# Performance work log

Hardware: AMD Instinct MI355X
Metric: run time of the kernel (lower is better)

## Reference

```python
import jax, jax.numpy as jnp
import numpy as np

NUM_EMBEDDINGS = 1024
EMBEDDING_DIM = 32  # Z_NH
COMMITMENT_LOSS_FACTOR = 0.1
QUANTIZATION_LOSS_FACTOR = 0.1


def setup_inputs() -> dict:
    key = jax.random.key(0)
    k1, k2 = jax.random.split(key)
    h = jax.random.normal(k1, (256, 512, EMBEDDING_DIM), dtype=jnp.float32)
    # nn.Embedding weight init: uniform(-1/K, 1/K)
    embeddings = jax.random.uniform(
        k2, (NUM_EMBEDDINGS, EMBEDDING_DIM), dtype=jnp.float32,
        minval=-1.0 / NUM_EMBEDDINGS, maxval=1.0 / NUM_EMBEDDINGS)
    return {"h": h, "embeddings": embeddings}


def reference(h, embeddings):
    flat = h.reshape(-1, EMBEDDING_DIM)                       # [N, D]
    dist = ((flat ** 2).sum(-1, keepdims=True)
            + (embeddings ** 2).sum(-1)
            - 2.0 * flat @ embeddings.T)                      # [N, K]
    idx = jnp.argmin(dist, axis=-1)                           # [N]
    # one_hot @ weight == direct row gather
    quantized = embeddings[idx].reshape(h.shape)              # [B, S, D]
    q_flat = quantized.reshape(-1, EMBEDDING_DIM)
    commitment_loss = jnp.mean((jax.lax.stop_gradient(q_flat) - flat) ** 2, axis=-1)
    embedding_loss = jnp.mean((q_flat - jax.lax.stop_gradient(flat)) ** 2, axis=-1)
    # straight-through estimator
    quantized_st = h + jax.lax.stop_gradient(quantized - h)
    loss = (commitment_loss * COMMITMENT_LOSS_FACTOR
            + embedding_loss * QUANTIZATION_LOSS_FACTOR)      # [N]
    quantized_indices = idx[:, None]                          # [N, 1]
    return quantized_st, quantized_indices, loss
```

## Files before the change

kernel.cpp:

```cpp
#include <hip/hip_runtime.h>


#define EMB_N 1024
#define DIM 32
#define NVEC (256 * 512)
#define NTILES (EMB_N / 16)
#define NT_LDS 36
#define MAXC 8

typedef unsigned long long u64;
typedef unsigned int u32;
typedef unsigned short ushortT;
typedef __attribute__((ext_vector_type(8))) short bf16x8;
typedef __attribute__((ext_vector_type(4))) float f32x4;

__device__ __forceinline__ u32 enc_f32(float x) {
    u32 u = __float_as_uint(x);
    return (u & 0x80000000u) ? ~u : (u | 0x80000000u);
}
__device__ __forceinline__ ushortT f2bf(float f) {
    u32 u = __float_as_uint(f);
    return (ushortT)((u + 0x7FFFu + ((u >> 16) & 1u)) >> 16);
}
__device__ __forceinline__ u64 shflx_u64(u64 x, int m) {
    int lo = __shfl_xor((int)(u32)x, m);
    int hi = __shfl_xor((int)(x >> 32), m);
    return ((u64)(u32)hi << 32) | (u32)lo;
}

__device__ __forceinline__ float norm2_np(const float* fr) {
    float sq[DIM];
#pragma unroll
    for (int i = 0; i < DIM; ++i) sq[i] = fr[i] * fr[i];
    float r[8];
#pragma unroll
    for (int j = 0; j < 8; ++j)
        r[j] = ((sq[j] + sq[j + 8]) + sq[j + 16]) + sq[j + 24];
    return ((r[0] + r[1]) + (r[2] + r[3])) + ((r[4] + r[5]) + (r[6] + r[7]));
}

__global__ __launch_bounds__(256) void prep_kernel(
    const float* __restrict__ emb, float* __restrict__ e2,
    ushortT* __restrict__ bfrag)
{
#pragma clang fp contract(off)
    const int t = blockIdx.x * 256 + threadIdx.x;
    const int l = t & 63;
    const int row = ((t >> 6) << 4) + (l & 15);
    const int k0 = (l >> 4) * 8;
    const float* ep = emb + (size_t)row * DIM + k0;
    ushortT* dst = bfrag + (size_t)t * 8;
#pragma unroll
    for (int j = 0; j < 8; ++j) dst[j] = f2bf(ep[j]);
    if (t < EMB_N) {
        const float* e = emb + (size_t)t * DIM;
        float tmp[DIM];
#pragma unroll
        for (int i = 0; i < DIM; ++i) tmp[i] = e[i];
        e2[t] = norm2_np(tmp);
    }
}

#define S1BODY(BEXPR) do {                                                      \
    bf16x8 b = *(const bf16x8*)(BEXPR);                                         \
    f32x4 d0 = __builtin_amdgcn_mfma_f32_16x16x32_bf16(afr0, b, zacc, 0, 0, 0); \
    f32x4 d1 = __builtin_amdgcn_mfma_f32_16x16x32_bf16(afr1, b, zacc, 0, 0, 0); \
    _Pragma("unroll")                                                           \
    for (int r = 0; r < 4; ++r) {                                               \
        bs[r]     = fmaxf(bs[r],     d0[r]);                                    \
        bs[4 + r] = fmaxf(bs[4 + r], d1[r]);                                    \
    }                                                                           \
} while (0)

#define S2BODY(BEXPR, NT) do {                                                  \
    bf16x8 b = *(const bf16x8*)(BEXPR);                                         \
    f32x4 d0 = __builtin_amdgcn_mfma_f32_16x16x32_bf16(afr0, b, zacc, 0, 0, 0); \
    f32x4 d1 = __builtin_amdgcn_mfma_f32_16x16x32_bf16(afr1, b, zacc, 0, 0, 0); \
    const u32 cc = (NT) * 16 + col16;                                           \
    bool q[8];                                                                  \
    bool any = false;                                                           \
    _Pragma("unroll")                                                           \
    for (int i = 0; i < 8; ++i) {                                               \
        float dv = ((i >> 2) ? d1[i & 3] : d0[i & 3]);                          \
        q[i] = (dv >= thr[i]);                                                  \
        any |= q[i];                                                            \
    }                                                                           \
    if (__ballot(any)) {                                                        \
        _Pragma("unroll")                                                       \
        for (int i = 0; i < 8; ++i) {                                           \
            if (__ballot(q[i])) {                                               \
                if (q[i]) {                                                     \
                    const int rloc = ((i >> 2) << 4) + quad * 4 + (i & 3);      \
                    u32 slot = atomicAdd(&cnt[rloc], 1u);                       \
                    if (slot < MAXC) cand[rloc * MAXC + slot] = (ushortT)cc;    \
                }                                                               \
            }                                                                   \
        }                                                                       \
    }                                                                           \
} while (0)

__global__ __launch_bounds__(256) void vq_scan(
    const float* __restrict__ h,
    const float* __restrict__ emb,
    const float* __restrict__ e2,
    const ushortT* __restrict__ bfrag,
    float* __restrict__ out_q, float* __restrict__ out_idx,
    float* __restrict__ out_loss)
{
#pragma clang fp contract(off)
    __shared__ __align__(16) ushortT s_b[NT_LDS * 512];
    __shared__ u32     lds_cnt[4][32];
    __shared__ ushortT lds_cand[4][32 * MAXC];

    {
        const uint4* src = (const uint4*)bfrag;
        uint4* dst = (uint4*)s_b;
        for (int o = threadIdx.x; o < NT_LDS * 64; o += 256) dst[o] = src[o];
    }

    const int wslot = threadIdx.x >> 6;
    const int wid   = (blockIdx.x * 256 + threadIdx.x) >> 6;
    const int lane  = threadIdx.x & 63;
    const int col16 = lane & 15;
    const int quad  = lane >> 4;
    const size_t row0 = (size_t)wid * 32;

    u32*     cnt  = lds_cnt[wslot];
    ushortT* cand = lds_cand[wslot];
    if (lane < 32) cnt[lane] = 0;

    bf16x8 afr0, afr1;
    float sa0, sa1;
    {
        const float* ap = h + (row0 + col16) * DIM + quad * 8;
        float4 x = *(const float4*)ap, y = *(const float4*)(ap + 4);
        afr0[0]=(short)f2bf(x.x); afr0[1]=(short)f2bf(x.y); afr0[2]=(short)f2bf(x.z); afr0[3]=(short)f2bf(x.w);
        afr0[4]=(short)f2bf(y.x); afr0[5]=(short)f2bf(y.y); afr0[6]=(short)f2bf(y.z); afr0[7]=(short)f2bf(y.w);
        sa0 = fabsf(x.x)+fabsf(x.y)+fabsf(x.z)+fabsf(x.w)+fabsf(y.x)+fabsf(y.y)+fabsf(y.z)+fabsf(y.w);
        const float* bp = ap + 16 * DIM;
        float4 u = *(const float4*)bp, v = *(const float4*)(bp + 4);
        afr1[0]=(short)f2bf(u.x); afr1[1]=(short)f2bf(u.y); afr1[2]=(short)f2bf(u.z); afr1[3]=(short)f2bf(u.w);
        afr1[4]=(short)f2bf(v.x); afr1[5]=(short)f2bf(v.y); afr1[6]=(short)f2bf(v.z); afr1[7]=(short)f2bf(v.w);
        sa1 = fabsf(u.x)+fabsf(u.y)+fabsf(u.z)+fabsf(u.w)+fabsf(v.x)+fabsf(v.y)+fabsf(v.z)+fabsf(v.w);
    }
    sa0 += __shfl_xor(sa0, 16); sa0 += __shfl_xor(sa0, 32);
    sa1 += __shfl_xor(sa1, 16); sa1 += __shfl_xor(sa1, 32);

    __syncthreads();

    const f32x4 zacc = {0.f, 0.f, 0.f, 0.f};

    float bs[8];
#pragma unroll
    for (int i = 0; i < 8; ++i) bs[i] = -3.4e38f;
#pragma unroll 2
    for (int nt = 0; nt < NT_LDS; ++nt)
        S1BODY(s_b + nt * 512 + lane * 8);
#pragma unroll 2
    for (int nt = NT_LDS; nt < NTILES; ++nt)
        S1BODY(bfrag + nt * 512 + lane * 8);
#pragma unroll
    for (int m = 1; m < 16; m <<= 1)
#pragma unroll
        for (int i = 0; i < 8; ++i) bs[i] = fmaxf(bs[i], __shfl_xor(bs[i], m));

    float thr[8];
#pragma unroll
    for (int i = 0; i < 8; ++i) {
        float sar = __shfl((i >> 2) ? sa1 : sa0, quad * 4 + (i & 3));
        thr[i] = bs[i] - __builtin_fmaf(sar, 0x1p-16f, 1.0e-4f);
    }

#pragma unroll 2
    for (int nt = 0; nt < NT_LDS; ++nt)
        S2BODY(s_b + nt * 512 + lane * 8, nt);
#pragma unroll 2
    for (int nt = NT_LDS; nt < NTILES; ++nt)
        S2BODY(bfrag + nt * 512 + lane * 8, nt);

    u64 ovf = __ballot((lane < 32) && (cnt[lane & 31] > MAXC));
    while (ovf) {
        const int r = (int)(__ffsll((unsigned long long)ovf) - 1);
        ovf &= ovf - 1;
        const float* fp = h + (row0 + r) * DIM;
        float fu[DIM];
#pragma unroll
        for (int i = 0; i < DIM; i += 4) {
            float4 x = *(const float4*)(fp + i);
            fu[i] = x.x; fu[i + 1] = x.y; fu[i + 2] = x.z; fu[i + 3] = x.w;
        }
        const float f2 = norm2_np(fu);
        u64 bk = ~0ull;
        for (int c = lane; c < EMB_N; c += 64) {
            const float* ep = emb + (size_t)c * DIM;
            float a = 0.f;
#pragma unroll
            for (int k = 0; k < DIM; ++k) a = __builtin_fmaf(fu[k], ep[k], a);
            float dd = (f2 + e2[c]) - (2.0f * a);
            u64 key = ((u64)enc_f32(dd) << 32) | (u32)c;
            if (key < bk) bk = key;
        }
#pragma unroll
        for (int m = 1; m < 64; m <<= 1) {
            u64 o = shflx_u64(bk, m);
            if (o < bk) bk = o;
        }
        if (lane == 0) { cand[r * MAXC] = (ushortT)(bk & 1023u); cnt[r] = 1; }
    }

    if (lane < 32) {
        const int row = (int)row0 + lane;
        const u32 n = cnt[lane];
        const float* f = h + (size_t)row * DIM;
        float fr[DIM];
#pragma unroll
        for (int i = 0; i < DIM; i += 4) {
            float4 x = *(const float4*)(f + i);
            fr[i] = x.x; fr[i + 1] = x.y; fr[i + 2] = x.z; fr[i + 3] = x.w;
        }
        int bidx;
        if (n == 1) {
            bidx = (int)cand[lane * MAXC];
        } else {
            const float f2 = norm2_np(fr);
            u64 best = ~0ull;
            for (u32 j = 0; j < n; ++j) {
                const u32 c = (u32)cand[lane * MAXC + j];
                const float* ep = emb + (size_t)c * DIM;
                float a = 0.f;
#pragma unroll
                for (int k = 0; k < DIM; ++k) a = __builtin_fmaf(fr[k], ep[k], a);
                float dd = (f2 + e2[c]) - (2.0f * a);
                u64 key = ((u64)enc_f32(dd) << 32) | c;
                if (key < best) best = key;
            }
            bidx = (int)(best & 0xFFFFFFFFu);
        }

        const float* qv = emb + (size_t)bidx * DIM;
        float ps = 0.f;
#pragma unroll
        for (int i = 0; i < DIM; i += 4) {
            float4 qx; qx.x = qv[i]; qx.y = qv[i+1]; qx.z = qv[i+2]; qx.w = qv[i+3];
            float dx = qx.x - fr[i], dy = qx.y - fr[i+1], dz = qx.z - fr[i+2], dw = qx.w - fr[i+3];
            ps += dx * dx; ps += dy * dy; ps += dz * dz; ps += dw * dw;
            float4 o;
            o.x = fr[i]     + (qx.x - fr[i]);
            o.y = fr[i + 1] + (qx.y - fr[i + 1]);
            o.z = fr[i + 2] + (qx.z - fr[i + 2]);
            o.w = fr[i + 3] + (qx.w - fr[i + 3]);
            *(float4*)(out_q + (size_t)row * DIM + i) = o;
        }
        float m = ps * (1.0f / DIM);
        out_idx[row]  = (float)bidx;
        out_loss[row] = m * 0.1f + m * 0.1f;
    }
}

__global__ void e2_kernel(const float* __restrict__ emb, float* __restrict__ e2) {
#pragma clang fp contract(off)
    int c = blockIdx.x * blockDim.x + threadIdx.x;
    if (c >= EMB_N) return;
    const float* e = emb + (size_t)c * DIM;
    float tmp[DIM];
#pragma unroll
    for (int i = 0; i < DIM; ++i) tmp[i] = e[i];
    e2[c] = norm2_np(tmp);
}

__global__ __launch_bounds__(256) void vq_kernel(
    const float* __restrict__ h, const float* __restrict__ emb,
    const float* __restrict__ e2, float* __restrict__ out_q,
    float* __restrict__ out_idx, float* __restrict__ out_loss)
{
#pragma clang fp contract(off)
    const int v = blockIdx.x * blockDim.x + threadIdx.x;
    const float* f = h + (size_t)v * DIM;
    float fr[DIM];
#pragma unroll
    for (int i = 0; i < DIM; i += 4) {
        float4 x = *(const float4*)(f + i);
        fr[i] = x.x; fr[i + 1] = x.y; fr[i + 2] = x.z; fr[i + 3] = x.w;
    }
    const float f2 = norm2_np(fr);
    float best = 3.4e38f; int bidx = 0;
#pragma unroll 1
    for (int c = 0; c < EMB_N; ++c) {
        const float* e = emb + (size_t)c * DIM;
        float a0 = 0.f;
#pragma unroll
        for (int k = 0; k < DIM; ++k) a0 = __builtin_fmaf(fr[k], e[k], a0);
        float d0 = (f2 + e2[c]) - (2.0f * a0);
        if (d0 < best) { best = d0; bidx = c; }
    }
    const float* q = emb + (size_t)bidx * DIM;
    float ps = 0.f;
#pragma unroll
    for (int i = 0; i < DIM; i += 4) {
        float4 qx; qx.x = q[i]; qx.y = q[i+1]; qx.z = q[i+2]; qx.w = q[i+3];
        float dx = qx.x - fr[i], dy = qx.y - fr[i+1], dz = qx.z - fr[i+2], dw = qx.w - fr[i+3];
        ps += dx * dx; ps += dy * dy; ps += dz * dz; ps += dw * dw;
        float4 o;
        o.x = fr[i] + (qx.x - fr[i]); o.y = fr[i+1] + (qx.y - fr[i+1]);
        o.z = fr[i+2] + (qx.z - fr[i+2]); o.w = fr[i+3] + (qx.w - fr[i+3]);
        *(float4*)(out_q + (size_t)v * DIM + i) = o;
    }
    float m = ps * (1.0f / DIM);
    out_idx[v]  = (float)bidx;
    out_loss[v] = m * 0.1f + m * 0.1f;
}

extern "C" void kernel_launch(void* const* d_in, const int* in_sizes, int n_in,
                              void* d_out, int out_size, void* d_ws, size_t ws_size,
                              hipStream_t stream) {
    const float* h   = (const float*)d_in[0];
    const float* emb = (const float*)d_in[1];
    float* out = (float*)d_out;
    float* out_q    = out;
    float* out_idx  = out + (size_t)NVEC * DIM;
    float* out_loss = out + (size_t)NVEC * DIM + NVEC;

    float*   e2    = (float*)d_ws;
    ushortT* bfrag = (ushortT*)((char*)d_ws + 4096);
    const size_t need = 4096 + (size_t)EMB_N * DIM * sizeof(ushortT);

    if (ws_size >= need) {
        prep_kernel<<<16, 256, 0, stream>>>(emb, e2, bfrag);
        vq_scan<<<1024, 256, 0, stream>>>(h, emb, e2, bfrag,
                                          out_q, out_idx, out_loss);
    } else {
        e2_kernel<<<EMB_N / 256, 256, 0, stream>>>(emb, e2);
        vq_kernel<<<NVEC / 256, 256, 0, stream>>>(h, emb, e2, out_q, out_idx, out_loss);
    }
}
```

Baseline: 126.2 us.

## Fuse two-pass MFMA scan into single pass with per-lane candidate bitmasks

Replaces the two full passes over the codebook (one to find each row's best similarity, one to recompute and collect near-best candidates) with a single pass. Each lane keeps a running max and bitmasks of tiles that beat a progressively tightened threshold, refreshed periodically by a cross-lane reduction. Global-memory B fragments are software-prefetched two tiles ahead. This halves the MFMA work and fragment loads, at the cost of more registers, a tighter margin constant, and possible extra candidates collected from early, looser thresholds.

```diff
diff --git a/kernel.cpp b/kernel.cpp
--- a/kernel.cpp
+++ b/kernel.cpp
@@ -61,42 +61,35 @@
     }
 }
 
-#define S1BODY(BEXPR) do {                                                      \
-    bf16x8 b = *(const bf16x8*)(BEXPR);                                         \
-    f32x4 d0 = __builtin_amdgcn_mfma_f32_16x16x32_bf16(afr0, b, zacc, 0, 0, 0); \
-    f32x4 d1 = __builtin_amdgcn_mfma_f32_16x16x32_bf16(afr1, b, zacc, 0, 0, 0); \
-    _Pragma("unroll")                                                           \
-    for (int r = 0; r < 4; ++r) {                                               \
-        bs[r]     = fmaxf(bs[r],     d0[r]);                                    \
-        bs[4 + r] = fmaxf(bs[4 + r], d1[r]);                                    \
-    }                                                                           \
+#define SBODY(BVAL, MASK, BIT) do {                                                 \
+    f32x4 d0 = __builtin_amdgcn_mfma_f32_16x16x32_bf16(afr0, (BVAL), zacc, 0, 0, 0);\
+    f32x4 d1 = __builtin_amdgcn_mfma_f32_16x16x32_bf16(afr1, (BVAL), zacc, 0, 0, 0);\
+    _Pragma("unroll")                                                               \
+    for (int i = 0; i < 8; ++i) {                                                   \
+        float dv = (i >> 2) ? d1[i & 3] : d0[i & 3];                                \
+        MASK[i] |= (dv >= thr_s[i]) ? (BIT) : 0u;                                   \
+        bsloc[i] = fmaxf(bsloc[i], dv);                                             \
+    }                                                                               \
 } while (0)
 
-#define S2BODY(BEXPR, NT) do {                                                  \
-    bf16x8 b = *(const bf16x8*)(BEXPR);                                         \
-    f32x4 d0 = __builtin_amdgcn_mfma_f32_16x16x32_bf16(afr0, b, zacc, 0, 0, 0); \
-    f32x4 d1 = __builtin_amdgcn_mfma_f32_16x16x32_bf16(afr1, b, zacc, 0, 0, 0); \
-    const u32 cc = (NT) * 16 + col16;                                           \
-    bool q[8];                                                                  \
-    bool any = false;                                                           \
-    _Pragma("unroll")                                                           \
-    for (int i = 0; i < 8; ++i) {                                               \
-        float dv = ((i >> 2) ? d1[i & 3] : d0[i & 3]);                          \
-        q[i] = (dv >= thr[i]);                                                  \
-        any |= q[i];                                                            \
-    }                                                                           \
-    if (__ballot(any)) {                                                        \
-        _Pragma("unroll")                                                       \
-        for (int i = 0; i < 8; ++i) {                                           \
-            if (__ballot(q[i])) {                                               \
-                if (q[i]) {                                                     \
-                    const int rloc = ((i >> 2) << 4) + quad * 4 + (i & 3);      \
-                    u32 slot = atomicAdd(&cnt[rloc], 1u);                       \
-                    if (slot < MAXC) cand[rloc * MAXC + slot] = (ushortT)cc;    \
-                }                                                               \
-            }                                                                   \
-        }                                                                       \
-    }                                                                           \
+#define SLDS(NT, MASK, BIT) do {                                                    \
+    bf16x8 bql = *(const bf16x8*)(s_b + (NT) * 512 + lane * 8);                     \
+    SBODY(bql, MASK, BIT);                                                          \
+} while (0)
+
+#define SHARE() do {                                                                \
+    _Pragma("unroll")                                                               \
+    for (int i = 0; i < 8; ++i) {                                                   \
+        float t_ = bsloc[i];                                                        \
+        t_ = fmaxf(t_, __shfl_xor(t_, 1));                                          \
+        t_ = fmaxf(t_, __shfl_xor(t_, 2));                                          \
+        t_ = fmaxf(t_, __shfl_xor(t_, 4));                                          \
+        t_ = fmaxf(t_, __shfl_xor(t_, 8));                                          \
+        thr_s[i] = t_ - mg[i];                                                      \
+        bool keep_ = (bsloc[i] >= thr_s[i]);                                        \
+        ml[i] = keep_ ? ml[i] : 0u;                                                 \
+        mh[i] = keep_ ? mh[i] : 0u;                                                 \
+    }                                                                               \
 } while (0)
 
 __global__ __launch_bounds__(256) void vq_scan(
@@ -150,33 +143,63 @@
 
     const f32x4 zacc = {0.f, 0.f, 0.f, 0.f};
 
-    float bs[8];
-#pragma unroll
-    for (int i = 0; i < 8; ++i) bs[i] = -3.4e38f;
-#pragma unroll 2
-    for (int nt = 0; nt < NT_LDS; ++nt)
-        S1BODY(s_b + nt * 512 + lane * 8);
-#pragma unroll 2
-    for (int nt = NT_LDS; nt < NTILES; ++nt)
-        S1BODY(bfrag + nt * 512 + lane * 8);
-#pragma unroll
-    for (int m = 1; m < 16; m <<= 1)
-#pragma unroll
-        for (int i = 0; i < 8; ++i) bs[i] = fmaxf(bs[i], __shfl_xor(bs[i], m));
-
-    float thr[8];
+    float bsloc[8], thr_s[8], mg[8];
+    u32 ml[8], mh[8];
 #pragma unroll
     for (int i = 0; i < 8; ++i) {
+        bsloc[i] = -3.4e38f; thr_s[i] = -3.4e38f; ml[i] = 0u; mh[i] = 0u;
         float sar = __shfl((i >> 2) ? sa1 : sa0, quad * 4 + (i & 3));
-        thr[i] = bs[i] - __builtin_fmaf(sar, 0x1p-16f, 1.0e-4f);
-    }
-
-#pragma unroll 2
-    for (int nt = 0; nt < NT_LDS; ++nt)
-        S2BODY(s_b + nt * 512 + lane * 8, nt);
-#pragma unroll 2
-    for (int nt = NT_LDS; nt < NTILES; ++nt)
-        S2BODY(bfrag + nt * 512 + lane * 8, nt);
+        mg[i] = __builtin_fmaf(sar, 0x1.8p-17f, 4.0e-5f);
+    }
+
+    SLDS(0, ml, 1u);
+    SHARE();
+#pragma unroll
+    for (int nt = 1; nt < 16; ++nt) SLDS(nt, ml, 1u << nt);
+    SHARE();
+#pragma unroll
+    for (int nt = 16; nt < 32; ++nt) SLDS(nt, ml, 1u << nt);
+    SHARE();
+#pragma unroll
+    for (int nt = 32; nt < NT_LDS; ++nt) SLDS(nt, mh, 1u << (nt - 32));
+
+    bf16x8 p0 = *(const bf16x8*)(bfrag + 36 * 512 + lane * 8);
+    bf16x8 p1 = *(const bf16x8*)(bfrag + 37 * 512 + lane * 8);
+#pragma unroll
+    for (int nt = 36; nt < 48; ++nt) {
+        bf16x8 nx = *(const bf16x8*)(bfrag + (nt + 2) * 512 + lane * 8);
+        SBODY(p0, mh, 1u << (nt - 32));
+        p0 = p1; p1 = nx;
+    }
+    SHARE();
+#pragma unroll
+    for (int nt = 48; nt < 62; ++nt) {
+        bf16x8 nx = *(const bf16x8*)(bfrag + (nt + 2) * 512 + lane * 8);
+        SBODY(p0, mh, 1u << (nt - 32));
+        p0 = p1; p1 = nx;
+    }
+    SBODY(p0, mh, 1u << 30);
+    SBODY(p1, mh, 1u << 31);
+    SHARE();
+
+#pragma unroll
+    for (int i = 0; i < 8; ++i) {
+        if (bsloc[i] >= thr_s[i]) {
+            const int rloc = ((i >> 2) << 4) + quad * 4 + (i & 3);
+            u32 m0 = ml[i];
+            while (m0) {
+                int b = __ffs(m0) - 1; m0 &= m0 - 1;
+                u32 slot = atomicAdd(&cnt[rloc], 1u);
+                if (slot < MAXC) cand[rloc * MAXC + slot] = (ushortT)((b << 4) + col16);
+            }
+            u32 m1 = mh[i];
+            while (m1) {
+                int b = __ffs(m1) - 1; m1 &= m1 - 1;
+                u32 slot = atomicAdd(&cnt[rloc], 1u);
+                if (slot < MAXC) cand[rloc * MAXC + slot] = (ushortT)(((b + 32) << 4) + col16);
+            }
+        }
+    }
 
     u64 ovf = __ballot((lane < 32) && (cnt[lane & 31] > MAXC));
     while (ovf) {
```

Result: slower. 177.1 us (+40.4%).

## Split codebook scan across wave pairs and tighten candidate threshold

Applied to the files above, without the earlier changes.

Each 32-row group is now handled by two waves that take alternating codebook tiles, doubling the block size to 512 threads. The per-row maxima from the first pass are combined through shared memory, so each wave's MFMA work halves and latency is spread over more waves. The candidate-pruning margin is also narrowed, which should produce fewer exact re-check candidates. The narrower margin risks missing the true argmin when bf16 error exceeds the new bound, and the extra barriers plus the idle second wave during finalization add some overhead.

```diff
diff --git a/kernel.cpp b/kernel.cpp
--- a/kernel.cpp
+++ b/kernel.cpp
@@ -76,7 +76,7 @@
     bf16x8 b = *(const bf16x8*)(BEXPR);                                         \
     f32x4 d0 = __builtin_amdgcn_mfma_f32_16x16x32_bf16(afr0, b, zacc, 0, 0, 0); \
     f32x4 d1 = __builtin_amdgcn_mfma_f32_16x16x32_bf16(afr1, b, zacc, 0, 0, 0); \
-    const u32 cc = (NT) * 16 + col16;                                           \
+    const u32 cc = (u32)(NT) * 16 + col16;                                      \
     bool q[8];                                                                  \
     bool any = false;                                                           \
     _Pragma("unroll")                                                           \
@@ -99,7 +99,7 @@
     }                                                                           \
 } while (0)
 
-__global__ __launch_bounds__(256) void vq_scan(
+__global__ __launch_bounds__(512, 8) void vq_scan(
     const float* __restrict__ h,
     const float* __restrict__ emb,
     const float* __restrict__ e2,
@@ -109,25 +109,27 @@
 {
 #pragma clang fp contract(off)
     __shared__ __align__(16) ushortT s_b[NT_LDS * 512];
+    __shared__ float   sm[8][32];
     __shared__ u32     lds_cnt[4][32];
     __shared__ ushortT lds_cand[4][32 * MAXC];
 
     {
         const uint4* src = (const uint4*)bfrag;
         uint4* dst = (uint4*)s_b;
-        for (int o = threadIdx.x; o < NT_LDS * 64; o += 256) dst[o] = src[o];
+        for (int o = threadIdx.x; o < NT_LDS * 64; o += 512) dst[o] = src[o];
     }
 
     const int wslot = threadIdx.x >> 6;
-    const int wid   = (blockIdx.x * 256 + threadIdx.x) >> 6;
+    const int pair  = wslot >> 1;
+    const int hh    = wslot & 1;
     const int lane  = threadIdx.x & 63;
     const int col16 = lane & 15;
     const int quad  = lane >> 4;
-    const size_t row0 = (size_t)wid * 32;
-
-    u32*     cnt  = lds_cnt[wslot];
-    ushortT* cand = lds_cand[wslot];
-    if (lane < 32) cnt[lane] = 0;
+    const size_t row0 = ((size_t)blockIdx.x * 4 + pair) * 32;
+
+    u32*     cnt  = lds_cnt[pair];
+    ushortT* cand = lds_cand[pair];
+    if (hh == 0 && lane < 32) cnt[lane] = 0;
 
     bf16x8 afr0, afr1;
     float sa0, sa1;
@@ -154,29 +156,50 @@
 #pragma unroll
     for (int i = 0; i < 8; ++i) bs[i] = -3.4e38f;
 #pragma unroll 2
-    for (int nt = 0; nt < NT_LDS; ++nt)
+    for (int k = 0; k < 18; ++k) {
+        const int nt = 2 * k + hh;
         S1BODY(s_b + nt * 512 + lane * 8);
+    }
 #pragma unroll 2
-    for (int nt = NT_LDS; nt < NTILES; ++nt)
-        S1BODY(bfrag + nt * 512 + lane * 8);
+    for (int k = 18; k < 32; ++k) {
+        const int nt = 2 * k + hh;
+        S1BODY(bfrag + (size_t)nt * 512 + lane * 8);
+    }
 #pragma unroll
     for (int m = 1; m < 16; m <<= 1)
 #pragma unroll
         for (int i = 0; i < 8; ++i) bs[i] = fmaxf(bs[i], __shfl_xor(bs[i], m));
 
+    if (col16 == 0) {
+#pragma unroll
+        for (int i = 0; i < 8; ++i)
+            sm[wslot][((i >> 2) << 4) + quad * 4 + (i & 3)] = bs[i];
+    }
+    __syncthreads();
+
     float thr[8];
 #pragma unroll
     for (int i = 0; i < 8; ++i) {
+        const int rloc = ((i >> 2) << 4) + quad * 4 + (i & 3);
+        float m = fmaxf(bs[i], sm[wslot ^ 1][rloc]);
         float sar = __shfl((i >> 2) ? sa1 : sa0, quad * 4 + (i & 3));
-        thr[i] = bs[i] - __builtin_fmaf(sar, 0x1p-16f, 1.0e-4f);
+        thr[i] = m - __builtin_fmaf(sar, 0x1.8p-17f, 4.0e-5f);
     }
 
 #pragma unroll 2
-    for (int nt = 0; nt < NT_LDS; ++nt)
+    for (int k = 0; k < 18; ++k) {
+        const int nt = 2 * k + hh;
         S2BODY(s_b + nt * 512 + lane * 8, nt);
+    }
 #pragma unroll 2
-    for (int nt = NT_LDS; nt < NTILES; ++nt)
-        S2BODY(bfrag + nt * 512 + lane * 8, nt);
+    for (int k = 18; k < 32; ++k) {
+        const int nt = 2 * k + hh;
+        S2BODY(bfrag + (size_t)nt * 512 + lane * 8, nt);
+    }
+
+    __syncthreads();
+
+    if (hh != 0) return;
 
     u64 ovf = __ballot((lane < 32) && (cnt[lane & 31] > MAXC));
     while (ovf) {
@@ -326,7 +349,7 @@
 
     if (ws_size >= need) {
         prep_kernel<<<16, 256, 0, stream>>>(emb, e2, bfrag);
-        vq_scan<<<1024, 256, 0, stream>>>(h, emb, e2, bfrag,
+        vq_scan<<<1024, 512, 0, stream>>>(h, emb, e2, bfrag,
                                           out_q, out_idx, out_loss);
     } else {
         e2_kernel<<<EMB_N / 256, 256, 0, stream>>>(emb, e2);
```

New measurement: 111.5 us. 11.7% less time.
